# Kernel optimization log

Measured on AMD Instinct MI355X. Metric: run time of the kernel, lower is better.

Reference implementation:

```python
import jax, jax.numpy as jnp
import numpy as np

B, N_V, N_H, K = 16384, 4096, 1024, 3
LR, MOMENTUM, WEIGHT_DECAY = 1e-3, 0.5, 1e-4


def setup_inputs() -> dict:
    key = jax.random.key(0)
    k1, k2, k3, k4 = jax.random.split(key, 4)
    inputs = jax.random.uniform(k1, (B, N_V), dtype=jnp.float32)
    weights = jax.random.normal(k2, (N_V, N_H), dtype=jnp.float32) * 0.1
    visible_bias = jnp.ones((N_V,), jnp.float32) * 0.5
    hidden_bias = jnp.zeros((N_H,), jnp.float32)
    weights_momentum = jnp.zeros((N_V, N_H), jnp.float32)
    visible_bias_momentum = jnp.zeros((N_V,), jnp.float32)
    hidden_bias_momentum = jnp.zeros((N_H,), jnp.float32)
    # one uniform vector of length n_hidden per sampling step (matches torch code)
    rand_h0 = jax.random.uniform(k3, (N_H,), dtype=jnp.float32)
    rand_hk = jax.random.uniform(k4, (K, N_H), dtype=jnp.float32)
    return {
        "inputs": inputs,
        "weights": weights,
        "visible_bias": visible_bias,
        "hidden_bias": hidden_bias,
        "weights_momentum": weights_momentum,
        "visible_bias_momentum": visible_bias_momentum,
        "hidden_bias_momentum": hidden_bias_momentum,
        "rand_h0": rand_h0,
        "rand_hk": rand_hk,
    }


def reference(inputs, weights, visible_bias, hidden_bias,
              weights_momentum, visible_bias_momentum, hidden_bias_momentum,
              rand_h0, rand_hk):
    dtype = inputs.dtype

    def sample_hidden(v):  # [B,V] -> [B,H]
        return jax.nn.sigmoid(v @ weights + hidden_bias)

    def sample_visible(h):  # [B,H] -> [B,V]
        return jax.nn.sigmoid(h @ weights.T + visible_bias)

    # positive phase
    pos_hidden_probs = sample_hidden(inputs)                      # [B,H]
    pos_hidden_acts = (pos_hidden_probs >= rand_h0).astype(dtype)  # [B,H]
    pos_associations = inputs.T @ pos_hidden_acts                 # [V,H]

    # negative phase (CD-k). NOTE: in the original torch code `hid_acts` is
    # never updated inside the k-1 loop, so every iteration recomputes the
    # identical visible_probs/hidden_probs from pos_hidden_acts; the extra
    # bernoulli draws (rand_hk) only feed hidden_acts, which is discarded.
    # The final values are therefore exactly one reconstruction step:
    neg_visible_probs = sample_visible(pos_hidden_acts)           # [B,V]
    neg_hidden_probs = sample_hidden(neg_visible_probs)           # [B,H]
    neg_associations = neg_visible_probs.T @ neg_hidden_probs     # [V,H]

    # momentum optimizer step
    batch_size = inputs.shape[0]
    w_mom = weights_momentum * MOMENTUM + (pos_associations - neg_associations)
    vb_mom = visible_bias_momentum * MOMENTUM + jnp.sum(inputs - neg_visible_probs, axis=0)
    hb_mom = hidden_bias_momentum * MOMENTUM + jnp.sum(pos_hidden_probs - neg_hidden_probs, axis=0)

    new_weights = weights + w_mom * (LR / batch_size)
    new_weights = new_weights - new_weights * WEIGHT_DECAY
    new_visible_bias = visible_bias + vb_mom * (LR / batch_size)
    new_hidden_bias = hidden_bias + hb_mom * (LR / batch_size)

    # reconstruction error (original has a bug using builtin `input`; intended `inputs`)
    error = jnp.sum((inputs - neg_visible_probs) ** 2)
    return (error, new_weights, new_visible_bias, new_hidden_bias)
```

## Files before the change

kernel.cpp:

```cpp
#include <hip/hip_runtime.h>
#include <hip/hip_bf16.h>

#define DEV __device__ __forceinline__

typedef __attribute__((ext_vector_type(8))) short bhalf8;
typedef __attribute__((ext_vector_type(4))) short bhalf4;
typedef __attribute__((ext_vector_type(4))) float floatx4;
typedef unsigned short ushort_t;

constexpr int NB = 16384;
constexpr int NV = 4096;
constexpr int NH = 1024;
constexpr float MOM = 0.5f;
constexpr float WD  = 1e-4f;
constexpr float LRB = 1e-3f / 16384.0f;

constexpr int BUF_SHORTS = 12288;
constexpr int LDS_SHORTS = 3 * BUF_SHORTS;
constexpr size_t LDS_BYTES = LDS_SHORTS * 2 + 64;

DEV unsigned short f2bf(float f) {
  unsigned u = __builtin_bit_cast(unsigned, f);
  u += 0x7FFFu + ((u >> 16) & 1u);
  return (unsigned short)(u >> 16);
}
DEV float bf2f(unsigned short u) {
  unsigned x = ((unsigned)u) << 16;
  return __builtin_bit_cast(float, x);
}
DEV float sigm(float x) { return 1.0f / (1.0f + __expf(-x)); }

DEV void gl16(const ushort_t* g, ushort_t* l) {
  __builtin_amdgcn_global_load_lds(
      (const __attribute__((address_space(1))) void*)g,
      (__attribute__((address_space(3))) void*)l,
      16, 0, 0);
}

__global__ void prep_cvt_t(const float* __restrict__ in,
                           ushort_t* __restrict__ obf,
                           ushort_t* __restrict__ oT, int R, int C) {
  __shared__ ushort_t t[64][72];
  const int c0 = blockIdx.x * 64, r0 = blockIdx.y * 64;
  const int tr = threadIdx.x >> 3, tc = (threadIdx.x & 7) * 8;
#pragma unroll
  for (int s = 0; s < 64; s += 32) {
    const float* p = in + (size_t)(r0 + tr + s) * C + c0 + tc;
    floatx4 lo = *(const floatx4*)p, hi = *(const floatx4*)(p + 4);
    bhalf8 r;
    r[0] = (short)f2bf(lo[0]); r[1] = (short)f2bf(lo[1]);
    r[2] = (short)f2bf(lo[2]); r[3] = (short)f2bf(lo[3]);
    r[4] = (short)f2bf(hi[0]); r[5] = (short)f2bf(hi[1]);
    r[6] = (short)f2bf(hi[2]); r[7] = (short)f2bf(hi[3]);
    *(bhalf8*)(obf + (size_t)(r0 + tr + s) * C + c0 + tc) = r;
    *(bhalf8*)&t[tr + s][tc] = r;
  }
  __syncthreads();
#pragma unroll
  for (int s = 0; s < 64; s += 32) {
    bhalf8 v;
#pragma unroll
    for (int j = 0; j < 8; ++j) v[j] = (short)t[tc + j][tr + s];
    *(bhalf8*)(oT + (size_t)(c0 + tr + s) * R + r0 + tc) = v;
  }
}

DEV void core(const ushort_t* __restrict__ Ap,
              const ushort_t* __restrict__ Bp,
              size_t ldA, size_t ldB, int nt,
              ushort_t* Lp, int wid, int lane, int wm, int wn,
              floatx4 (&acc)[8][4]) {
  const int lr = lane & 15, kg = lane >> 4;
  const int sslot = ((lane & 3) ^ (((lane & 32) ? 2 : 0) | ((lane & 8) ? 1 : 0))) * 8;
  const ushort_t* gA = Ap + (size_t)(wid * 16 + (lane >> 2)) * ldA + sslot;
  const ushort_t* gB = Bp + (size_t)(wid * 16 + (lane >> 2)) * ldB + sslot;
  const int rslot = ((kg ^ (((lr & 8) ? 2 : 0) | ((lr & 2) ? 1 : 0))) * 8);
  const int aoff = (wm * 128 + lr) * 32 + rslot;
  const int boff = 8192 + (wn * 64 + lr) * 32 + rslot;

  auto stage = [&](int buf, int t) {
    const ushort_t* a = gA + (size_t)t * 32;
    const ushort_t* b = gB + (size_t)t * 32;
    ushort_t* LA = Lp + buf * BUF_SHORTS + wid * 512;
    ushort_t* LB = LA + 8192;
#pragma unroll
    for (int i = 0; i < 4; ++i) gl16(a + (size_t)(i * 64) * ldA, LA + i * 2048);
#pragma unroll
    for (int i = 0; i < 2; ++i) gl16(b + (size_t)(i * 64) * ldB, LB + i * 2048);
  };

  stage(0, 0);
  stage(1, 1);
  int cur = 0, pre = 2;
  for (int t = 0; t < nt; ++t) {
    if (t + 1 < nt) asm volatile("s_waitcnt vmcnt(6)" ::: "memory");
    else            asm volatile("s_waitcnt vmcnt(0)" ::: "memory");
    asm volatile("s_barrier" ::: "memory");
    if (t + 2 < nt) stage(pre, t + 2);
    const ushort_t* aB = Lp + cur * BUF_SHORTS + aoff;
    const ushort_t* bB = Lp + cur * BUF_SHORTS + boff;
    bhalf8 fa[8], fb[4];
#pragma unroll
    for (int m = 0; m < 8; ++m) fa[m] = *(const bhalf8*)(aB + m * 512);
#pragma unroll
    for (int n = 0; n < 4; ++n) fb[n] = *(const bhalf8*)(bB + n * 512);
    asm volatile("s_waitcnt lgkmcnt(0)" ::: "memory");
    __builtin_amdgcn_sched_barrier(0);
    __builtin_amdgcn_s_setprio(1);
#pragma unroll
    for (int m = 0; m < 8; ++m)
#pragma unroll
      for (int n = 0; n < 4; ++n)
        acc[m][n] = __builtin_amdgcn_mfma_f32_16x16x32_bf16(fa[m], fb[n], acc[m][n], 0, 0, 0);
    __builtin_amdgcn_s_setprio(0);
    if (++cur == 3) cur = 0;
    if (++pre == 3) pre = 0;
  }
}

template <int MODE>
__global__ __launch_bounds__(256, 2)
void gemm_fused256(const ushort_t* __restrict__ Ab,
                   const ushort_t* __restrict__ Bb,
                   int N, int K,
                   const float* __restrict__ bias,
                   const float* __restrict__ rand_h0,
                   ushort_t* __restrict__ Pout,
                   ushort_t* __restrict__ PoutT,
                   float* __restrict__ colsum,
                   const ushort_t* __restrict__ inbf,
                   float* __restrict__ err_accum) {
  extern __shared__ ushort_t Lsh[];
  const int tid = threadIdx.x;
  const int wid = tid >> 6, lane = tid & 63;
  const int wm = wid >> 1, wn = wid & 1;
  const int lr = lane & 15, kg = lane >> 4;

  const int nwg = gridDim.x * gridDim.y;
  const int id = blockIdx.y * gridDim.x + blockIdx.x;
  const int sid = (id & 7) * (nwg >> 3) + (id >> 3);
  const int n0 = (sid % gridDim.x) * 128;
  const int m0 = (sid / gridDim.x) * 256;

  floatx4 acc[8][4] = {};
  core(Ab + (size_t)m0 * K, Bb + (size_t)n0 * K, K, K, K / 32,
       Lsh, wid, lane, wm, wn, acc);

  float esum = 0.0f;
#pragma unroll
  for (int ni = 0; ni < 4; ++ni) {
    const int col = n0 + wn * 64 + ni * 16 + lr;
    const float b = bias[col];
    const float r0 = (MODE == 0) ? rand_h0[col] : 0.0f;
    float cs = 0.0f;
#pragma unroll
    for (int mi = 0; mi < 8; ++mi) {
      const int rowb = m0 + wm * 128 + mi * 16 + kg * 4;
      bhalf4 tp;
#pragma unroll
      for (int r = 0; r < 4; ++r) {
        const float p = sigm(acc[mi][ni][r] + b);
        ushort_t ov;
        if (MODE == 0) {
          cs += p;
          ov = (p >= r0) ? (ushort_t)0x3F80u : (ushort_t)0u;
          Pout[(size_t)(rowb + r) * N + col] = ov;
        } else if (MODE == 1) {
          ov = f2bf(p);
          Pout[(size_t)(rowb + r) * N + col] = ov;
          const float d = bf2f(inbf[(size_t)(rowb + r) * N + col]) - p;
          cs += d;
          esum += d * d;
        } else {
          cs += p;
          ov = f2bf(p);
        }
        tp[r] = (short)ov;
      }
      *(bhalf4*)&PoutT[(size_t)col * NB + rowb] = tp;
    }
    cs += __shfl_xor(cs, 16);
    cs += __shfl_xor(cs, 32);
    if (kg == 0) atomicAdd(&colsum[col], cs);
  }
  if (MODE == 1) {
    float* ered = (float*)(Lsh + LDS_SHORTS);
    esum += __shfl_xor(esum, 1);
    esum += __shfl_xor(esum, 2);
    esum += __shfl_xor(esum, 4);
    esum += __shfl_xor(esum, 8);
    esum += __shfl_xor(esum, 16);
    esum += __shfl_xor(esum, 32);
    __syncthreads();
    if (lane == 0) ered[wid] = esum;
    __syncthreads();
    if (tid == 0) atomicAdd(err_accum, ered[0] + ered[1] + ered[2] + ered[3]);
  }
}

__global__ __launch_bounds__(256, 2)
void gemm_nt_dual(const ushort_t* __restrict__ A1, const ushort_t* __restrict__ B1,
                  const ushort_t* __restrict__ A2, const ushort_t* __restrict__ B2,
                  float* __restrict__ outd) {
  extern __shared__ ushort_t Lsh[];
  const int tid = threadIdx.x;
  const int wid = tid >> 6, lane = tid & 63;
  const int wm = wid >> 1, wn = wid & 1;
  const int lr = lane & 15, kg = lane >> 4;

  const int bid = blockIdx.x;
  const int r = bid & 127;
  const int m0 = (r & 15) * 256;
  const int n0 = (r >> 4) * 128;
  const int z  = bid >> 7;
  const size_t kb0 = (size_t)z * (NB / 4);
  constexpr int NT = (NB / 4) / 32;

  floatx4 acc[8][4] = {};
  core(A1 + (size_t)m0 * NB + kb0, B1 + (size_t)n0 * NB + kb0, NB, NB, NT,
       Lsh, wid, lane, wm, wn, acc);
#pragma unroll
  for (int m = 0; m < 8; ++m)
#pragma unroll
    for (int n = 0; n < 4; ++n)
#pragma unroll
      for (int j = 0; j < 4; ++j) acc[m][n][j] = -acc[m][n][j];
  core(A2 + (size_t)m0 * NB + kb0, B2 + (size_t)n0 * NB + kb0, NB, NB, NT,
       Lsh, wid, lane, wm, wn, acc);
  float* od = outd + (size_t)z * NV * NH;
#pragma unroll
  for (int mi = 0; mi < 8; ++mi) {
    const int rowb = m0 + wm * 128 + mi * 16 + kg * 4;
#pragma unroll
    for (int ni = 0; ni < 4; ++ni) {
      const int col = n0 + wn * 64 + ni * 16 + lr;
#pragma unroll
      for (int r2 = 0; r2 < 4; ++r2)
        od[(size_t)(rowb + r2) * NH + col] = -acc[mi][ni][r2];
    }
  }
}

__global__ void wupdate_kernel(const float* __restrict__ W, const float* __restrict__ wm,
                               const float* __restrict__ diff, float* __restrict__ outW) {
  const int i = blockIdx.x * blockDim.x + threadIdx.x;
  constexpr size_t SL = (size_t)NV * NH / 4;
  const floatx4 w = ((const floatx4*)W)[i];
  const floatx4 m = ((const floatx4*)wm)[i];
  const floatx4 a = ((const floatx4*)diff)[i];
  const floatx4 b = ((const floatx4*)diff)[i + SL];
  const floatx4 c = ((const floatx4*)diff)[i + 2 * SL];
  const floatx4 d = ((const floatx4*)diff)[i + 3 * SL];
  floatx4 o;
#pragma unroll
  for (int j = 0; j < 4; ++j)
    o[j] = (w[j] + (m[j] * MOM + (a[j] + b[j]) + (c[j] + d[j])) * LRB) * (1.0f - WD);
  ((floatx4*)outW)[i] = o;
}

__global__ void biaserr_kernel(const float* __restrict__ vb, const float* __restrict__ vbm,
                               const float* __restrict__ vbcs,
                               const float* __restrict__ hb, const float* __restrict__ hbm,
                               const float* __restrict__ phpcs, const float* __restrict__ nhpcs,
                               const float* __restrict__ err, float* __restrict__ out) {
  const int i = blockIdx.x * blockDim.x + threadIdx.x;
  if (i < NV) out[1 + (size_t)NV * NH + i] = vb[i] + (vbm[i] * MOM + vbcs[i]) * LRB;
  if (i < NH) out[1 + (size_t)NV * NH + NV + i] = hb[i] + (hbm[i] * MOM + (phpcs[i] - nhpcs[i])) * LRB;
  if (i == 0) out[0] = err[0];
}

extern "C" void kernel_launch(void* const* d_in, const int* in_sizes, int n_in,
                              void* d_out, int out_size, void* d_ws, size_t ws_size,
                              hipStream_t stream) {
  const float* inputs  = (const float*)d_in[0];
  const float* W       = (const float*)d_in[1];
  const float* vb      = (const float*)d_in[2];
  const float* hb      = (const float*)d_in[3];
  const float* wmom    = (const float*)d_in[4];
  const float* vbmom   = (const float*)d_in[5];
  const float* hbmom   = (const float*)d_in[6];
  const float* rand_h0 = (const float*)d_in[7];

  hipFuncSetAttribute((const void*)gemm_fused256<0>, hipFuncAttributeMaxDynamicSharedMemorySize, (int)LDS_BYTES);
  hipFuncSetAttribute((const void*)gemm_fused256<1>, hipFuncAttributeMaxDynamicSharedMemorySize, (int)LDS_BYTES);
  hipFuncSetAttribute((const void*)gemm_fused256<2>, hipFuncAttributeMaxDynamicSharedMemorySize, (int)LDS_BYTES);
  hipFuncSetAttribute((const void*)gemm_nt_dual, hipFuncAttributeMaxDynamicSharedMemorySize, (int)LDS_BYTES);

  char* ws = (char*)d_ws;
  size_t off = 0;
  auto take = [&](size_t b) { size_t r = off; off = (off + b + 1023) & ~(size_t)1023; return r; };
  ushort_t* Wbf   = (ushort_t*)(ws + take((size_t)NV * NH * 2));
  ushort_t* WT    = (ushort_t*)(ws + take((size_t)NV * NH * 2));
  ushort_t* inbf  = (ushort_t*)(ws + take((size_t)NB * NV * 2));
  ushort_t* inT   = (ushort_t*)(ws + take((size_t)NB * NV * 2));
  ushort_t* nvp   = (ushort_t*)(ws + take((size_t)NB * NV * 2));
  ushort_t* nvpT  = (ushort_t*)(ws + take((size_t)NB * NV * 2));
  ushort_t* acts  = (ushort_t*)(ws + take((size_t)NB * NH * 2));
  ushort_t* actsT = (ushort_t*)(ws + take((size_t)NB * NH * 2));
  ushort_t* nhpT  = (ushort_t*)(ws + take((size_t)NB * NH * 2));
  const size_t red_bytes = (size_t)(NH + NH + NV + 64) * 4;
  float* phpcs = (float*)(ws + take(red_bytes));
  float* nhpcs = phpcs + NH;
  float* vbcs  = nhpcs + NH;
  float* errp  = vbcs + NV;

  float* diff = (float*)inbf;

  hipMemsetAsync(phpcs, 0, red_bytes, stream);

  prep_cvt_t<<<dim3(NV / 64, NB / 64), 256, 0, stream>>>(inputs, inbf, inT, NB, NV);
  prep_cvt_t<<<dim3(NH / 64, NV / 64), 256, 0, stream>>>(W, Wbf, WT, NV, NH);

  gemm_fused256<0><<<dim3(NH / 128, NB / 256), 256, LDS_BYTES, stream>>>(
      inbf, WT, NH, NV, hb, rand_h0, acts, actsT, phpcs, nullptr, nullptr);

  gemm_fused256<1><<<dim3(NV / 128, NB / 256), 256, LDS_BYTES, stream>>>(
      acts, Wbf, NV, NH, vb, nullptr, nvp, nvpT, vbcs, inbf, errp);

  gemm_fused256<2><<<dim3(NH / 128, NB / 256), 256, LDS_BYTES, stream>>>(
      nvp, WT, NH, NV, hb, nullptr, nullptr, nhpT, nhpcs, nullptr, nullptr);

  gemm_nt_dual<<<dim3(512), 256, LDS_BYTES, stream>>>(inT, actsT, nvpT, nhpT, diff);

  wupdate_kernel<<<dim3((NV * NH / 4) / 256), 256, 0, stream>>>(W, wmom, diff, (float*)d_out + 1);
  biaserr_kernel<<<dim3(16), 256, 0, stream>>>(vb, vbmom, vbcs, hb, hbmom, phpcs, nhpcs, errp,
                                               (float*)d_out);
}
```

Baseline: 1.143 ms.

## Stage GEMM epilogue tiles through LDS and move transposes to separate kernels

The fused GEMM epilogue now writes its output tile to LDS and then emits coalesced 16-byte row stores, instead of doing scattered 2-byte row stores plus 8-byte transposed stores. The transposed copies are produced by separate LDS transpose kernels that run after each GEMM. The visible-bias column sum is split into an input column sum, computed during the prep conversion, and a reconstruction column sum. The error term is now computed from the bf16-rounded probabilities. This removes uncoalesced global writes from the epilogue at the cost of three extra kernel launches and an additional read and write of each activation matrix.

```diff
diff --git a/kernel.cpp b/kernel.cpp
--- a/kernel.cpp
+++ b/kernel.cpp
@@ -4,7 +4,6 @@
 #define DEV __device__ __forceinline__
 
 typedef __attribute__((ext_vector_type(8))) short bhalf8;
-typedef __attribute__((ext_vector_type(4))) short bhalf4;
 typedef __attribute__((ext_vector_type(4))) float floatx4;
 typedef unsigned short ushort_t;
 
@@ -39,10 +38,12 @@
 
 __global__ void prep_cvt_t(const float* __restrict__ in,
                            ushort_t* __restrict__ obf,
-                           ushort_t* __restrict__ oT, int R, int C) {
+                           ushort_t* __restrict__ oT, int R, int C,
+                           float* __restrict__ csum) {
   __shared__ ushort_t t[64][72];
   const int c0 = blockIdx.x * 64, r0 = blockIdx.y * 64;
   const int tr = threadIdx.x >> 3, tc = (threadIdx.x & 7) * 8;
+  float ps[8] = {};
 #pragma unroll
   for (int s = 0; s < 64; s += 32) {
     const float* p = in + (size_t)(r0 + tr + s) * C + c0 + tc;
@@ -52,9 +53,26 @@
     r[2] = (short)f2bf(lo[2]); r[3] = (short)f2bf(lo[3]);
     r[4] = (short)f2bf(hi[0]); r[5] = (short)f2bf(hi[1]);
     r[6] = (short)f2bf(hi[2]); r[7] = (short)f2bf(hi[3]);
+    if (csum) {
+#pragma unroll
+      for (int j = 0; j < 4; ++j) { ps[j] += lo[j]; ps[4 + j] += hi[j]; }
+    }
     *(bhalf8*)(obf + (size_t)(r0 + tr + s) * C + c0 + tc) = r;
     *(bhalf8*)&t[tr + s][tc] = r;
   }
+  if (csum) {
+#pragma unroll
+    for (int j = 0; j < 8; ++j) {
+      ps[j] += __shfl_xor(ps[j], 8);
+      ps[j] += __shfl_xor(ps[j], 16);
+      ps[j] += __shfl_xor(ps[j], 32);
+    }
+    const int lane = threadIdx.x & 63;
+    if (lane < 8) {
+#pragma unroll
+      for (int j = 0; j < 8; ++j) atomicAdd(&csum[c0 + lane * 8 + j], ps[j]);
+    }
+  }
   __syncthreads();
 #pragma unroll
   for (int s = 0; s < 64; s += 32) {
@@ -62,6 +80,26 @@
 #pragma unroll
     for (int j = 0; j < 8; ++j) v[j] = (short)t[tc + j][tr + s];
     *(bhalf8*)(oT + (size_t)(c0 + tr + s) * R + r0 + tc) = v;
+  }
+}
+
+__global__ void transb(const ushort_t* __restrict__ in,
+                       ushort_t* __restrict__ out, int R, int C) {
+  __shared__ ushort_t t[64][72];
+  const int c0 = blockIdx.x * 64, r0 = blockIdx.y * 64;
+  const int tr = threadIdx.x >> 3, tc = (threadIdx.x & 7) * 8;
+#pragma unroll
+  for (int s = 0; s < 64; s += 32) {
+    bhalf8 v = *(const bhalf8*)(in + (size_t)(r0 + tr + s) * C + c0 + tc);
+    *(bhalf8*)&t[tr + s][tc] = v;
+  }
+  __syncthreads();
+#pragma unroll
+  for (int s = 0; s < 64; s += 32) {
+    bhalf8 v;
+#pragma unroll
+    for (int j = 0; j < 8; ++j) v[j] = (short)t[tc + j][tr + s];
+    *(bhalf8*)(out + (size_t)(c0 + tr + s) * R + r0 + tc) = v;
   }
 }
 
@@ -126,7 +164,6 @@
                    const float* __restrict__ bias,
                    const float* __restrict__ rand_h0,
                    ushort_t* __restrict__ Pout,
-                   ushort_t* __restrict__ PoutT,
                    float* __restrict__ colsum,
                    const ushort_t* __restrict__ inbf,
                    float* __restrict__ err_accum) {
@@ -146,42 +183,50 @@
   core(Ab + (size_t)m0 * K, Bb + (size_t)n0 * K, K, K, K / 32,
        Lsh, wid, lane, wm, wn, acc);
 
-  float esum = 0.0f;
+  __syncthreads();
+  ushort_t* Rt = Lsh;
 #pragma unroll
   for (int ni = 0; ni < 4; ++ni) {
-    const int col = n0 + wn * 64 + ni * 16 + lr;
+    const int lcol = wn * 64 + ni * 16 + lr;
+    const int col = n0 + lcol;
     const float b = bias[col];
     const float r0 = (MODE == 0) ? rand_h0[col] : 0.0f;
     float cs = 0.0f;
 #pragma unroll
     for (int mi = 0; mi < 8; ++mi) {
-      const int rowb = m0 + wm * 128 + mi * 16 + kg * 4;
-      bhalf4 tp;
+      const int lrow = wm * 128 + mi * 16 + kg * 4;
 #pragma unroll
       for (int r = 0; r < 4; ++r) {
         const float p = sigm(acc[mi][ni][r] + b);
+        cs += p;
         ushort_t ov;
-        if (MODE == 0) {
-          cs += p;
-          ov = (p >= r0) ? (ushort_t)0x3F80u : (ushort_t)0u;
-          Pout[(size_t)(rowb + r) * N + col] = ov;
-        } else if (MODE == 1) {
-          ov = f2bf(p);
-          Pout[(size_t)(rowb + r) * N + col] = ov;
-          const float d = bf2f(inbf[(size_t)(rowb + r) * N + col]) - p;
-          cs += d;
-          esum += d * d;
-        } else {
-          cs += p;
-          ov = f2bf(p);
-        }
-        tp[r] = (short)ov;
+        if (MODE == 0) ov = (p >= r0) ? (ushort_t)0x3F80u : (ushort_t)0u;
+        else           ov = f2bf(p);
+        Rt[(lrow + r) * 132 + lcol] = ov;
       }
-      *(bhalf4*)&PoutT[(size_t)col * NB + rowb] = tp;
     }
     cs += __shfl_xor(cs, 16);
     cs += __shfl_xor(cs, 32);
     if (kg == 0) atomicAdd(&colsum[col], cs);
+  }
+  __syncthreads();
+  float esum = 0.0f;
+  const int c8 = (tid & 15) * 8;
+  const int rb = tid >> 4;
+#pragma unroll
+  for (int it = 0; it < 16; ++it) {
+    const int lrow = it * 16 + rb;
+    bhalf8 v = *(const bhalf8*)&Rt[lrow * 132 + c8];
+    const size_t g = (size_t)(m0 + lrow) * N + n0 + c8;
+    *(bhalf8*)&Pout[g] = v;
+    if (MODE == 1) {
+      bhalf8 iv = *(const bhalf8*)&inbf[g];
+#pragma unroll
+      for (int j = 0; j < 8; ++j) {
+        const float d = bf2f((ushort_t)iv[j]) - bf2f((ushort_t)v[j]);
+        esum += d * d;
+      }
+    }
   }
   if (MODE == 1) {
     float* ered = (float*)(Lsh + LDS_SHORTS);
@@ -191,7 +236,6 @@
     esum += __shfl_xor(esum, 8);
     esum += __shfl_xor(esum, 16);
     esum += __shfl_xor(esum, 32);
-    __syncthreads();
     if (lane == 0) ered[wid] = esum;
     __syncthreads();
     if (tid == 0) atomicAdd(err_accum, ered[0] + ered[1] + ered[2] + ered[3]);
@@ -219,6 +263,7 @@
   floatx4 acc[8][4] = {};
   core(A1 + (size_t)m0 * NB + kb0, B1 + (size_t)n0 * NB + kb0, NB, NB, NT,
        Lsh, wid, lane, wm, wn, acc);
+  __syncthreads();
 #pragma unroll
   for (int m = 0; m < 8; ++m)
 #pragma unroll
@@ -259,13 +304,15 @@
 }
 
 __global__ void biaserr_kernel(const float* __restrict__ vb, const float* __restrict__ vbm,
-                               const float* __restrict__ vbcs,
+                               const float* __restrict__ incs, const float* __restrict__ nvpcs,
                                const float* __restrict__ hb, const float* __restrict__ hbm,
                                const float* __restrict__ phpcs, const float* __restrict__ nhpcs,
                                const float* __restrict__ err, float* __restrict__ out) {
   const int i = blockIdx.x * blockDim.x + threadIdx.x;
-  if (i < NV) out[1 + (size_t)NV * NH + i] = vb[i] + (vbm[i] * MOM + vbcs[i]) * LRB;
-  if (i < NH) out[1 + (size_t)NV * NH + NV + i] = hb[i] + (hbm[i] * MOM + (phpcs[i] - nhpcs[i])) * LRB;
+  if (i < NV) out[1 + (size_t)NV * NH + i] =
+      vb[i] + (vbm[i] * MOM + (incs[i] - nvpcs[i])) * LRB;
+  if (i < NH) out[1 + (size_t)NV * NH + NV + i] =
+      hb[i] + (hbm[i] * MOM + (phpcs[i] - nhpcs[i])) * LRB;
   if (i == 0) out[0] = err[0];
 }
 
@@ -298,31 +345,36 @@
   ushort_t* acts  = (ushort_t*)(ws + take((size_t)NB * NH * 2));
   ushort_t* actsT = (ushort_t*)(ws + take((size_t)NB * NH * 2));
   ushort_t* nhpT  = (ushort_t*)(ws + take((size_t)NB * NH * 2));
-  const size_t red_bytes = (size_t)(NH + NH + NV + 64) * 4;
+  const size_t red_bytes = (size_t)(NH + NH + NV + NV + 64) * 4;
   float* phpcs = (float*)(ws + take(red_bytes));
   float* nhpcs = phpcs + NH;
-  float* vbcs  = nhpcs + NH;
-  float* errp  = vbcs + NV;
-
-  float* diff = (float*)inbf;
+  float* incs  = nhpcs + NH;
+  float* nvpcs = incs + NV;
+  float* errp  = nvpcs + NV;
+
+  ushort_t* nhp = acts;
+  float* diff   = (float*)inbf;
 
   hipMemsetAsync(phpcs, 0, red_bytes, stream);
 
-  prep_cvt_t<<<dim3(NV / 64, NB / 64), 256, 0, stream>>>(inputs, inbf, inT, NB, NV);
-  prep_cvt_t<<<dim3(NH / 64, NV / 64), 256, 0, stream>>>(W, Wbf, WT, NV, NH);
+  prep_cvt_t<<<dim3(NV / 64, NB / 64), 256, 0, stream>>>(inputs, inbf, inT, NB, NV, incs);
+  prep_cvt_t<<<dim3(NH / 64, NV / 64), 256, 0, stream>>>(W, Wbf, WT, NV, NH, nullptr);
 
   gemm_fused256<0><<<dim3(NH / 128, NB / 256), 256, LDS_BYTES, stream>>>(
-      inbf, WT, NH, NV, hb, rand_h0, acts, actsT, phpcs, nullptr, nullptr);
+      inbf, WT, NH, NV, hb, rand_h0, acts, phpcs, nullptr, nullptr);
+  transb<<<dim3(NH / 64, NB / 64), 256, 0, stream>>>(acts, actsT, NB, NH);
 
   gemm_fused256<1><<<dim3(NV / 128, NB / 256), 256, LDS_BYTES, stream>>>(
-      acts, Wbf, NV, NH, vb, nullptr, nvp, nvpT, vbcs, inbf, errp);
+      acts, Wbf, NV, NH, vb, nullptr, nvp, nvpcs, inbf, errp);
+  transb<<<dim3(NV / 64, NB / 64), 256, 0, stream>>>(nvp, nvpT, NB, NV);
 
   gemm_fused256<2><<<dim3(NH / 128, NB / 256), 256, LDS_BYTES, stream>>>(
-      nvp, WT, NH, NV, hb, nullptr, nullptr, nhpT, nhpcs, nullptr, nullptr);
+      nvp, WT, NH, NV, hb, nullptr, nhp, nhpcs, nullptr, nullptr);
+  transb<<<dim3(NH / 64, NB / 64), 256, 0, stream>>>(nhp, nhpT, NB, NH);
 
   gemm_nt_dual<<<dim3(512), 256, LDS_BYTES, stream>>>(inT, actsT, nvpT, nhpT, diff);
 
   wupdate_kernel<<<dim3((NV * NH / 4) / 256), 256, 0, stream>>>(W, wmom, diff, (float*)d_out + 1);
-  biaserr_kernel<<<dim3(16), 256, 0, stream>>>(vb, vbmom, vbcs, hb, hbmom, phpcs, nhpcs, errp,
-                                               (float*)d_out);
-}
+  biaserr_kernel<<<dim3(16), 256, 0, stream>>>(vb, vbmom, incs, nvpcs, hb, hbmom,
+                                               phpcs, nhpcs, errp, (float*)d_out);
+}
```

Measured after the change: 1.172 ms. 1.02x slower.
